# Optimization experiments

Measured on AMD Instinct MI355X. Metric: run time of the kernel, lower is better.

Reference implementation:

```python
import jax, jax.numpy as jnp
import numpy as np

VOCAB = 1276   # medical-code vocab (one_hot depth for word)
AGE_DEPTH = 91 # one_hot depth for age


def setup_inputs() -> dict:
    key = jax.random.key(0)
    k1, k2, k3 = jax.random.split(key, 3)
    B, S, BAG, D = 64, 128, 40, 768
    word = jax.random.randint(k1, (B, S, BAG), 0, VOCAB)
    age = jax.random.randint(k2, (B, S), 0, AGE_DEPTH)
    W = jax.random.normal(k3, (VOCAB + AGE_DEPTH, D), dtype=jnp.float32) * 0.02
    b = jnp.zeros((D,), dtype=jnp.float32)
    return {"word": word, "age": age, "W": W, "b": b}


def reference(word, age, W, b):
    # word: [B, S, BAG] int codes; age: [B, S] int.
    B, S, BAG = word.shape
    # Multi-hot count-sum: equivalent to reduce_sum(one_hot(word, VOCAB), axis=-2)
    # but computed via scatter-add, avoiding the dense [B,S,BAG,VOCAB] tensor.
    flat = word.reshape(B * S, BAG)
    offs = jnp.arange(B * S, dtype=word.dtype)[:, None] * VOCAB
    counts = (
        jnp.zeros((B * S * VOCAB,), jnp.float32)
        .at[(flat + offs).ravel()]
        .add(1.0)
        .reshape(B, S, VOCAB)
    )
    year = jax.nn.one_hot(age, AGE_DEPTH, dtype=jnp.float32)  # [B, S, 91]
    x = jnp.concatenate([counts, year], axis=-1)              # [B, S, 1367]
    return x @ W + b                                          # [B, S, 768]
```

## Files before the change

### kernel.cpp

```cpp
#include <hip/hip_runtime.h>
#include <hip/hip_fp16.h>

constexpr int BAG       = 40;
constexpr int D         = 768;
constexpr int VOCAB     = 1276;
constexpr int AGE_DEPTH = 91;
constexpr int WROWS     = VOCAB + AGE_DEPTH;

constexpr int COLS   = 16;
constexpr int NSLICE = D / COLS;
constexpr int RPB    = 256;
constexpr int TPB    = 512;
constexpr int NCHUNK = COLS / 8;
constexpr int LDSU   = NCHUNK * WROWS;

typedef float fx4 __attribute__((ext_vector_type(4)));

__device__ __forceinline__ __half2 u2h(uint u) {
    union { uint u; __half2 h; } v; v.u = u; return v.h;
}
__device__ __forceinline__ ushort f2h(float f) {
    __half h = __float2half(f);
    return *reinterpret_cast<ushort*>(&h);
}

__global__ __launch_bounds__(TPB) void embed_lds_kernel(
    const int* __restrict__ word,
    const int* __restrict__ age,
    const float* __restrict__ W,
    const float* __restrict__ bias,
    float* __restrict__ out)
{
    __shared__ uint4 lds4[LDSU];

    const int rb    = blockIdx.x;
    const int slice = blockIdx.y;
    const int c0    = slice * COLS;

    const int t     = threadIdx.x;
    const int chunk = t & 1;
    const int rloc  = t >> 1;
    const int row   = rb * RPB + rloc;

    const int* __restrict__ wrow = word + row * BAG;
    int idx[BAG];
    #pragma unroll
    for (int j = 0; j < BAG; j += 4) {
        const int4 q = *reinterpret_cast<const int4*>(wrow + j);
        idx[j] = q.x; idx[j + 1] = q.y; idx[j + 2] = q.z; idx[j + 3] = q.w;
    }
    const int aidx = VOCAB + age[row];

    for (int s = t; s < LDSU; s += TPB) {
        const int r = s >> 1;
        const int u = s & 1;
        const float* src = W + (size_t)r * D + c0 + u * 8;
        const float4 a = *reinterpret_cast<const float4*>(src);
        const float4 b = *reinterpret_cast<const float4*>(src + 4);
        uint4 p;
        p.x = (uint)f2h(a.x) | ((uint)f2h(a.y) << 16);
        p.y = (uint)f2h(a.z) | ((uint)f2h(a.w) << 16);
        p.z = (uint)f2h(b.x) | ((uint)f2h(b.y) << 16);
        p.w = (uint)f2h(b.z) | ((uint)f2h(b.w) << 16);
        lds4[u * WROWS + r] = p;
    }

    __syncthreads();

    const uint4* __restrict__ lp = lds4 + chunk * WROWS;

    __half2 acc0 = u2h(0u), acc1 = u2h(0u), acc2 = u2h(0u), acc3 = u2h(0u);
    #pragma unroll
    for (int j = 0; j < BAG; ++j) {
        const uint4 g = lp[idx[j]];
        acc0 = __hadd2(acc0, u2h(g.x));
        acc1 = __hadd2(acc1, u2h(g.y));
        acc2 = __hadd2(acc2, u2h(g.z));
        acc3 = __hadd2(acc3, u2h(g.w));
    }
    {
        const uint4 g = lp[aidx];
        acc0 = __hadd2(acc0, u2h(g.x));
        acc1 = __hadd2(acc1, u2h(g.y));
        acc2 = __hadd2(acc2, u2h(g.z));
        acc3 = __hadd2(acc3, u2h(g.w));
    }

    const float* bp = bias + c0 + chunk * 8;
    const float4 b0 = *reinterpret_cast<const float4*>(bp);
    const float4 b1 = *reinterpret_cast<const float4*>(bp + 4);
    fx4 o0 = { b0.x + __low2float(acc0), b0.y + __high2float(acc0),
               b0.z + __low2float(acc1), b0.w + __high2float(acc1) };
    fx4 o1 = { b1.x + __low2float(acc2), b1.y + __high2float(acc2),
               b1.z + __low2float(acc3), b1.w + __high2float(acc3) };
    float* op = out + (size_t)row * D + c0 + chunk * 8;
    __builtin_nontemporal_store(o0, reinterpret_cast<fx4*>(op));
    __builtin_nontemporal_store(o1, reinterpret_cast<fx4*>(op + 4));
}

__global__ __launch_bounds__(192) void embedbag_f32_kernel(
    const int* __restrict__ word, const int* __restrict__ age,
    const float* __restrict__ W, const float* __restrict__ bias,
    float* __restrict__ out)
{
    const int row = blockIdx.x;
    const int c   = threadIdx.x * 4;

    float4 acc = *reinterpret_cast<const float4*>(&bias[c]);
    const int* __restrict__ wrow = word + row * BAG;

    #pragma unroll 8
    for (int j = 0; j < BAG; ++j) {
        const int idx = wrow[j];
        const float4 v = *reinterpret_cast<const float4*>(&W[(size_t)idx * D + c]);
        acc.x += v.x; acc.y += v.y; acc.z += v.z; acc.w += v.w;
    }
    {
        const int idx = VOCAB + age[row];
        const float4 v = *reinterpret_cast<const float4*>(&W[(size_t)idx * D + c]);
        acc.x += v.x; acc.y += v.y; acc.z += v.z; acc.w += v.w;
    }
    *reinterpret_cast<float4*>(&out[(size_t)row * D + c]) = acc;
}

extern "C" void kernel_launch(void* const* d_in, const int* in_sizes, int n_in,
                              void* d_out, int out_size, void* d_ws, size_t ws_size,
                              hipStream_t stream) {
    const int* word   = (const int*)d_in[0];
    const int* age    = (const int*)d_in[1];
    const float* W    = (const float*)d_in[2];
    const float* bias = (const float*)d_in[3];
    float* out        = (float*)d_out;

    const int rows = in_sizes[1];

    if (rows % RPB == 0) {
        dim3 grid(rows / RPB, NSLICE);
        embed_lds_kernel<<<grid, TPB, 0, stream>>>(word, age, W, bias, out);
    } else {
        embedbag_f32_kernel<<<rows, D / 4, 0, stream>>>(word, age, W, bias, out);
    }
}
```

Before: 27.47 us.

## Pre-convert W to fp16 and split columns between LDS and global gathers

```diff
diff --git a/kernel.cpp b/kernel.cpp
--- a/kernel.cpp
+++ b/kernel.cpp
@@ -7,12 +7,11 @@
 constexpr int AGE_DEPTH = 91;
 constexpr int WROWS     = VOCAB + AGE_DEPTH;
 
-constexpr int COLS   = 16;
-constexpr int NSLICE = D / COLS;
-constexpr int RPB    = 256;
-constexpr int TPB    = 512;
-constexpr int NCHUNK = COLS / 8;
-constexpr int LDSU   = NCHUNK * WROWS;
+constexpr int CPB  = 32;
+constexpr int NSLC = D / CPB;
+constexpr int RPB  = 256;
+constexpr int TPB  = 512;
+constexpr int LDSU = 2 * WROWS;
 
 typedef float fx4 __attribute__((ext_vector_type(4)));
 
@@ -24,18 +23,32 @@
     return *reinterpret_cast<ushort*>(&h);
 }
 
-__global__ __launch_bounds__(TPB) void embed_lds_kernel(
+__global__ __launch_bounds__(256) void convert_w_f16(
+    const float* __restrict__ W, ushort* __restrict__ Wh, int n)
+{
+    const int i = (blockIdx.x * 256 + threadIdx.x) * 8;
+    if (i + 8 > n) return;
+    const float4 a = *reinterpret_cast<const float4*>(W + i);
+    const float4 b = *reinterpret_cast<const float4*>(W + i + 4);
+    uint4 p;
+    p.x = (uint)f2h(a.x) | ((uint)f2h(a.y) << 16);
+    p.y = (uint)f2h(a.z) | ((uint)f2h(a.w) << 16);
+    p.z = (uint)f2h(b.x) | ((uint)f2h(b.y) << 16);
+    p.w = (uint)f2h(b.z) | ((uint)f2h(b.w) << 16);
+    *reinterpret_cast<uint4*>(Wh + i) = p;
+}
+
+__global__ __launch_bounds__(TPB) void embed_hybrid_kernel(
     const int* __restrict__ word,
     const int* __restrict__ age,
-    const float* __restrict__ W,
+    const ushort* __restrict__ Wh,
     const float* __restrict__ bias,
     float* __restrict__ out)
 {
     __shared__ uint4 lds4[LDSU];
 
-    const int rb    = blockIdx.x;
-    const int slice = blockIdx.y;
-    const int c0    = slice * COLS;
+    const int rb = blockIdx.x;
+    const int c0 = blockIdx.y * CPB;
 
     const int t     = threadIdx.x;
     const int chunk = t & 1;
@@ -43,59 +56,87 @@
     const int row   = rb * RPB + rloc;
 
     const int* __restrict__ wrow = word + row * BAG;
-    int idx[BAG];
-    #pragma unroll
-    for (int j = 0; j < BAG; j += 4) {
-        const int4 q = *reinterpret_cast<const int4*>(wrow + j);
-        idx[j] = q.x; idx[j + 1] = q.y; idx[j + 2] = q.z; idx[j + 3] = q.w;
-    }
     const int aidx = VOCAB + age[row];
 
     for (int s = t; s < LDSU; s += TPB) {
         const int r = s >> 1;
         const int u = s & 1;
-        const float* src = W + (size_t)r * D + c0 + u * 8;
-        const float4 a = *reinterpret_cast<const float4*>(src);
-        const float4 b = *reinterpret_cast<const float4*>(src + 4);
-        uint4 p;
-        p.x = (uint)f2h(a.x) | ((uint)f2h(a.y) << 16);
-        p.y = (uint)f2h(a.z) | ((uint)f2h(a.w) << 16);
-        p.z = (uint)f2h(b.x) | ((uint)f2h(b.y) << 16);
-        p.w = (uint)f2h(b.z) | ((uint)f2h(b.w) << 16);
-        lds4[u * WROWS + r] = p;
+        lds4[u * WROWS + r] =
+            *reinterpret_cast<const uint4*>(Wh + (size_t)r * D + c0 + u * 8);
+    }
+    __syncthreads();
+
+    const uint4*  __restrict__ lpL = lds4 + chunk * WROWS;
+    const ushort* __restrict__ gpG = Wh + c0 + 16 + chunk * 8;
+
+    __half2 aL0 = u2h(0u), aL1 = u2h(0u), aL2 = u2h(0u), aL3 = u2h(0u);
+    __half2 aG0 = u2h(0u), aG1 = u2h(0u), aG2 = u2h(0u), aG3 = u2h(0u);
+
+    #pragma unroll
+    for (int jb = 0; jb < BAG; jb += 8) {
+        const int4 q0 = *reinterpret_cast<const int4*>(wrow + jb);
+        const int4 q1 = *reinterpret_cast<const int4*>(wrow + jb + 4);
+        const int id[8] = {q0.x, q0.y, q0.z, q0.w, q1.x, q1.y, q1.z, q1.w};
+
+        uint4 g[8];
+        #pragma unroll
+        for (int u = 0; u < 8; ++u)
+            g[u] = *reinterpret_cast<const uint4*>(gpG + (size_t)id[u] * D);
+
+        #pragma unroll
+        for (int u = 0; u < 8; ++u) {
+            const uint4 l = lpL[id[u]];
+            aL0 = __hadd2(aL0, u2h(l.x));
+            aL1 = __hadd2(aL1, u2h(l.y));
+            aL2 = __hadd2(aL2, u2h(l.z));
+            aL3 = __hadd2(aL3, u2h(l.w));
+        }
+
+        #pragma unroll
+        for (int u = 0; u < 8; ++u) {
+            aG0 = __hadd2(aG0, u2h(g[u].x));
+            aG1 = __hadd2(aG1, u2h(g[u].y));
+            aG2 = __hadd2(aG2, u2h(g[u].z));
+            aG3 = __hadd2(aG3, u2h(g[u].w));
+        }
     }
 
-    __syncthreads();
-
-    const uint4* __restrict__ lp = lds4 + chunk * WROWS;
-
-    __half2 acc0 = u2h(0u), acc1 = u2h(0u), acc2 = u2h(0u), acc3 = u2h(0u);
-    #pragma unroll
-    for (int j = 0; j < BAG; ++j) {
-        const uint4 g = lp[idx[j]];
-        acc0 = __hadd2(acc0, u2h(g.x));
-        acc1 = __hadd2(acc1, u2h(g.y));
-        acc2 = __hadd2(acc2, u2h(g.z));
-        acc3 = __hadd2(acc3, u2h(g.w));
-    }
     {
-        const uint4 g = lp[aidx];
-        acc0 = __hadd2(acc0, u2h(g.x));
-        acc1 = __hadd2(acc1, u2h(g.y));
-        acc2 = __hadd2(acc2, u2h(g.z));
-        acc3 = __hadd2(acc3, u2h(g.w));
+        const uint4 g = *reinterpret_cast<const uint4*>(gpG + (size_t)aidx * D);
+        const uint4 l = lpL[aidx];
+        aL0 = __hadd2(aL0, u2h(l.x));
+        aL1 = __hadd2(aL1, u2h(l.y));
+        aL2 = __hadd2(aL2, u2h(l.z));
+        aL3 = __hadd2(aL3, u2h(l.w));
+        aG0 = __hadd2(aG0, u2h(g.x));
+        aG1 = __hadd2(aG1, u2h(g.y));
+        aG2 = __hadd2(aG2, u2h(g.z));
+        aG3 = __hadd2(aG3, u2h(g.w));
     }
 
-    const float* bp = bias + c0 + chunk * 8;
-    const float4 b0 = *reinterpret_cast<const float4*>(bp);
-    const float4 b1 = *reinterpret_cast<const float4*>(bp + 4);
-    fx4 o0 = { b0.x + __low2float(acc0), b0.y + __high2float(acc0),
-               b0.z + __low2float(acc1), b0.w + __high2float(acc1) };
-    fx4 o1 = { b1.x + __low2float(acc2), b1.y + __high2float(acc2),
-               b1.z + __low2float(acc3), b1.w + __high2float(acc3) };
-    float* op = out + (size_t)row * D + c0 + chunk * 8;
-    __builtin_nontemporal_store(o0, reinterpret_cast<fx4*>(op));
-    __builtin_nontemporal_store(o1, reinterpret_cast<fx4*>(op + 4));
+    const int cL = c0 + chunk * 8;
+    const int cG = c0 + 16 + chunk * 8;
+    float* opL = out + (size_t)row * D + cL;
+    float* opG = out + (size_t)row * D + cG;
+
+    const float4 bL0 = *reinterpret_cast<const float4*>(bias + cL);
+    const float4 bL1 = *reinterpret_cast<const float4*>(bias + cL + 4);
+    const float4 bG0 = *reinterpret_cast<const float4*>(bias + cG);
+    const float4 bG1 = *reinterpret_cast<const float4*>(bias + cG + 4);
+
+    fx4 oL0 = { bL0.x + __low2float(aL0), bL0.y + __high2float(aL0),
+                bL0.z + __low2float(aL1), bL0.w + __high2float(aL1) };
+    fx4 oL1 = { bL1.x + __low2float(aL2), bL1.y + __high2float(aL2),
+                bL1.z + __low2float(aL3), bL1.w + __high2float(aL3) };
+    fx4 oG0 = { bG0.x + __low2float(aG0), bG0.y + __high2float(aG0),
+                bG0.z + __low2float(aG1), bG0.w + __high2float(aG1) };
+    fx4 oG1 = { bG1.x + __low2float(aG2), bG1.y + __high2float(aG2),
+                bG1.z + __low2float(aG3), bG1.w + __high2float(aG3) };
+
+    __builtin_nontemporal_store(oL0, reinterpret_cast<fx4*>(opL));
+    __builtin_nontemporal_store(oL1, reinterpret_cast<fx4*>(opL + 4));
+    __builtin_nontemporal_store(oG0, reinterpret_cast<fx4*>(opG));
+    __builtin_nontemporal_store(oG1, reinterpret_cast<fx4*>(opG + 4));
 }
 
 __global__ __launch_bounds__(192) void embedbag_f32_kernel(
@@ -134,9 +175,14 @@
 
     const int rows = in_sizes[1];
 
-    if (rows % RPB == 0) {
-        dim3 grid(rows / RPB, NSLICE);
-        embed_lds_kernel<<<grid, TPB, 0, stream>>>(word, age, W, bias, out);
+    const size_t need = (size_t)WROWS * D * sizeof(ushort);
+    if (rows % RPB == 0 && ws_size >= need) {
+        ushort* Wh = (ushort*)d_ws;
+        const int n = WROWS * D;
+        convert_w_f16<<<(n / 8 + 255) / 256, 256, 0, stream>>>(W, Wh, n);
+        dim3 grid(rows / RPB, NSLC);
+        embed_hybrid_kernel<<<grid, TPB, 0, stream>>>(
+            word, age, (const ushort*)Wh, bias, out);
     } else {
         embedbag_f32_kernel<<<rows, D / 4, 0, stream>>>(word, age, W, bias, out);
     }
```

New measurement: 50.20 us. 1.83x slower.
